# Kernel optimization log

Measured on AMD Instinct MI355X. Metric: run time of the kernel, lower is better.

## Reference

```python
import jax, jax.numpy as jnp
import numpy as np
from jax import lax

# Architecture constants (match init_kwargs)
B = 4          # clips
T_SEG = 8      # num_segments
D_IN = 256
D_HID = 64
H = 112
W = 112
WIN_T = 5      # window[0], temporal
WIN_S = 9      # window[1] == window[2], spatial
MAXD = WIN_S // 2


def setup_inputs() -> dict:
    key = jax.random.key(0)
    k1, k2, k3, k4 = jax.random.split(key, 4)
    x = jax.random.normal(k1, (B * T_SEG, D_IN, H, W), jnp.float32)
    conv_w = jax.random.normal(k2, (D_HID, D_IN, 3, 3), jnp.float32) * 0.05
    bn_gamma = jnp.ones((D_HID,), jnp.float32)
    bn_beta = jnp.zeros((D_HID,), jnp.float32)
    bn_mean = jax.random.normal(k3, (D_HID,), jnp.float32) * 0.1
    bn_var = jax.random.uniform(k4, (D_HID,), jnp.float32, minval=0.5, maxval=1.5)
    return {"x": x, "conv_w": conv_w, "bn_gamma": bn_gamma, "bn_beta": bn_beta,
            "bn_mean": bn_mean, "bn_var": bn_var}


def reference(x, conv_w, bn_gamma, bn_beta, bn_mean, bn_var):
    # downsample: Conv2d(k=3, s=2, p=1, no bias) + BatchNorm2d (eval) + ReLU
    y = lax.conv_general_dilated(x, conv_w, window_strides=(2, 2),
                                 padding=((1, 1), (1, 1)),
                                 dimension_numbers=("NCHW", "OIHW", "NCHW"))
    scale = bn_gamma / jnp.sqrt(bn_var + 1e-5)
    y = jax.nn.relu((y - bn_mean[:, None, None]) * scale[:, None, None]
                    + bn_beta[:, None, None])
    bt, c, h, w = y.shape
    b = bt // T_SEG
    y = y.reshape(b, T_SEG, c, h, w)
    # per-frame, per-pixel L2 normalization over channels (eps=1e-6, as in _L2normalize)
    yn = y / jnp.sqrt(jnp.sum(y * y, axis=2, keepdims=True) + 1e-6)
    # temporal zero-pad (padded frames normalize to 0 in the original too: 0/sqrt(eps)=0)
    half_t = WIN_T // 2
    ypad = jnp.pad(yn, ((0, 0), (half_t, half_t), (0, 0), (0, 0), (0, 0)))
    # spatial zero-pad by max displacement
    ypad = jnp.pad(ypad, ((0, 0), (0, 0), (0, 0), (MAXD, MAXD), (MAXD, MAXD)))
    # temporal windows: f2[b, t, l] = padded frame t+l   -> (b, T, L, c, h+2m, w+2m)
    f2 = jnp.stack([ypad[:, l:l + T_SEG] for l in range(WIN_T)], axis=2)
    # local windowed correlation (equivalent to einsum + _corr_abs_to_rel):
    # out[b,t,l,u,v,h,w] = sum_c yn[b,t,c,h,w] * f2[b,t,l,c,h+u,w+v]
    corrs = []
    for u in range(WIN_S):
        for v in range(WIN_S):
            corrs.append(jnp.einsum("btchw,btlchw->btlhw",
                                     yn, f2[:, :, :, :, u:u + h, v:v + w]))
    corr = jnp.stack(corrs, axis=-1).reshape(b, T_SEG, WIN_T, h, w, WIN_S, WIN_S)
    # '(b t l) u v h w -> b t h w 1 l u v'
    corr = jnp.transpose(corr, (0, 1, 3, 4, 2, 5, 6))
    return corr[:, :, :, :, None, :, :, :]
```

## Files before the change

### kernel.cpp

```cpp
#include <hip/hip_runtime.h>
#include <hip/hip_bf16.h>

#define TSEG 8
#define NBC 4
#define NBT 32
#define CIN 256
#define CH 64
#define HIN 112
#define WIN_ 112
#define HO 56
#define WO 56
#define HPD 64
#define WPD 64

#define FRSZE ((size_t)(HPD * WPD * CH))
#define ZF_U   147456
#define FR_U   (ZF_U + 262144)
#define WS_TOTAL_BYTES ((size_t)(FR_U + 32 * 262144) * 2)

typedef __attribute__((ext_vector_type(8))) short bf16x8;
typedef __attribute__((ext_vector_type(4))) float f32x4;

__device__ __forceinline__ unsigned short f2bf(float f) {
    union { float f; unsigned u; } c; c.f = f;
    unsigned u = c.u + 0x7fffu + ((c.u >> 16) & 1u);
    return (unsigned short)(u >> 16);
}

__global__ __launch_bounds__(256) void wprep_k(
    const float* __restrict__ w, unsigned short* __restrict__ wpp)
{
    int e = blockIdx.x * 256 + threadIdx.x;
    int cout = e / 2304;
    int rem  = e - cout * 2304;
    int ci   = rem / 9;
    int tap  = rem - ci * 9;
    wpp[((size_t)tap * 64 + cout) * 256 + ci] = f2bf(w[e]);
}

__global__ __launch_bounds__(256) void conv_mfma_k(
    const float* __restrict__ x, const unsigned short* __restrict__ wpp,
    const float* __restrict__ gamma, const float* __restrict__ beta,
    const float* __restrict__ mean, const float* __restrict__ var,
    unsigned short* __restrict__ frames)
{
    __shared__ unsigned short in_lds[5 * 120 * 32];
    __shared__ float sq[2][2][64];

    const int tid  = threadIdx.x;
    const int lane = tid & 63;
    const int wv   = tid >> 6;
    const int r    = wv >> 1;
    const int nh   = wv & 1;
    const int l15  = lane & 15;
    const int l4   = lane >> 4;
    const int hb   = blockIdx.x;
    const int bt   = blockIdx.y;

    const float* xb = x + (size_t)bt * (CIN * HIN * WIN_);

    f32x4 acc[4][2];
#pragma unroll
    for (int mt = 0; mt < 4; ++mt) {
        acc[mt][0] = (f32x4){0.f, 0.f, 0.f, 0.f};
        acc[mt][1] = (f32x4){0.f, 0.f, 0.f, 0.f};
    }

    int a_off[4][3];
#pragma unroll
    for (int mt = 0; mt < 4; ++mt) {
        int c = mt * 16 + l15; if (c > 55) c = 55;
#pragma unroll
        for (int kw = 0; kw < 3; ++kw) {
            int col = 2 * c + kw;
            int ba  = col * 64 + l4 * 16;
            ba ^= ((col >> 1) & 7) << 4;
            a_off[mt][kw] = ba;
        }
    }

    const unsigned short* bptr0 = wpp + ((size_t)(nh * 32 + l15) * 256 + l4 * 8);
    const unsigned short* bptr1 = wpp + ((size_t)(nh * 32 + 16 + l15) * 256 + l4 * 8);

    const int ih0 = 4 * hb - 1;

    for (int cb = 0; cb < 8; ++cb) {
        __syncthreads();
#pragma unroll
        for (int j = 0; j < 5; ++j) {
            const int jj  = wv + j * 4;
            const int row = jj >> 2, cig = jj & 3;
            const int ih  = ih0 + row;
            const int ihc = ih < 0 ? 0 : (ih > 111 ? 111 : ih);
            const float* xr = xb + ((size_t)(cb * 32 + cig * 8) * HIN + ihc) * WIN_;
            const bool rowin = (ih >= 0) && (ih < HIN);
#pragma unroll
            for (int p = 0; p < 2; ++p) {
                const int col = lane + p * 64;
                if (col < 113) {
                    const int iw  = col - 1;
                    const int iwc = iw < 0 ? 0 : iw;
                    const bool inb = rowin && (iw >= 0);
                    unsigned pk[4];
#pragma unroll
                    for (int q = 0; q < 4; ++q) {
                        float v0 = xr[(size_t)(2 * q) * HIN * WIN_ + iwc];
                        float v1 = xr[(size_t)(2 * q + 1) * HIN * WIN_ + iwc];
                        v0 = inb ? v0 : 0.f;
                        v1 = inb ? v1 : 0.f;
                        union { float f; unsigned u; } c0, c1; c0.f = v0; c1.f = v1;
                        unsigned u0 = c0.u + 0x7fffu + ((c0.u >> 16) & 1u);
                        unsigned u1 = c1.u + 0x7fffu + ((c1.u >> 16) & 1u);
                        pk[q] = (u0 >> 16) | (u1 & 0xffff0000u);
                    }
                    int ba = (row * 120 + col) * 64 + cig * 16;
                    ba ^= ((col >> 1) & 7) << 4;
                    *(uint4*)((char*)in_lds + ba) = make_uint4(pk[0], pk[1], pk[2], pk[3]);
                }
            }
        }
        __syncthreads();

        const int rowb = (2 * r) * 7680;
#pragma unroll
        for (int kh = 0; kh < 3; ++kh) {
            const int rb = rowb + kh * 7680;
#pragma unroll
            for (int kw = 0; kw < 3; ++kw) {
                const int tap = kh * 3 + kw;
                const bf16x8 bf0 = *(const bf16x8*)(bptr0 + tap * 16384 + cb * 32);
                const bf16x8 bf1 = *(const bf16x8*)(bptr1 + tap * 16384 + cb * 32);
#pragma unroll
                for (int mt = 0; mt < 4; ++mt) {
                    const bf16x8 af = *(const bf16x8*)((const char*)in_lds + (rb + a_off[mt][kw]));
                    acc[mt][0] = __builtin_amdgcn_mfma_f32_16x16x32_bf16(af, bf0, acc[mt][0], 0, 0, 0);
                    acc[mt][1] = __builtin_amdgcn_mfma_f32_16x16x32_bf16(af, bf1, acc[mt][1], 0, 0, 0);
                }
            }
        }
    }

    const int cout0 = nh * 32 + l15;
    const int cout1 = cout0 + 16;
    const float sc0 = gamma[cout0] * rsqrtf(var[cout0] + 1e-5f);
    const float bb0 = beta[cout0] - mean[cout0] * sc0;
    const float sc1 = gamma[cout1] * rsqrtf(var[cout1] + 1e-5f);
    const float bb1 = beta[cout1] - mean[cout1] * sc1;

    float yv[4][2][4];
    float ssr[4][4];
#pragma unroll
    for (int mt = 0; mt < 4; ++mt) {
#pragma unroll
        for (int reg = 0; reg < 4; ++reg) {
            float y0 = fmaxf(fmaf(acc[mt][0][reg], sc0, bb0), 0.f);
            float y1 = fmaxf(fmaf(acc[mt][1][reg], sc1, bb1), 0.f);
            yv[mt][0][reg] = y0; yv[mt][1][reg] = y1;
            float ss = y0 * y0 + y1 * y1;
            ss += __shfl_xor(ss, 1);
            ss += __shfl_xor(ss, 2);
            ss += __shfl_xor(ss, 4);
            ss += __shfl_xor(ss, 8);
            ssr[mt][reg] = ss;
        }
    }
    if (l15 == 0) {
#pragma unroll
        for (int mt = 0; mt < 4; ++mt)
#pragma unroll
            for (int reg = 0; reg < 4; ++reg)
                sq[r][nh][mt * 16 + l4 * 4 + reg] = ssr[mt][reg];
    }
    __syncthreads();

    const int h = 2 * hb + r;
    unsigned short* fdst = frames + (size_t)bt * FRSZE + (size_t)(h + 4) * WPD * CH;
#pragma unroll
    for (int mt = 0; mt < 4; ++mt) {
#pragma unroll
        for (int reg = 0; reg < 4; ++reg) {
            const int c = mt * 16 + l4 * 4 + reg;
            if (c < 56) {
                const float tot = sq[r][0][c] + sq[r][1][c];
                const float inv = rsqrtf(tot + 1e-6f);
                unsigned short* dp = fdst + (size_t)(c + 4) * CH;
                dp[cout0] = f2bf(yv[mt][0][reg] * inv);
                dp[cout1] = f2bf(yv[mt][1][reg] * inv);
            }
        }
    }
}

__global__ __launch_bounds__(64) void corr_mfma_k(
    const unsigned short* __restrict__ frames, float* __restrict__ out)
{
    __shared__ float so[56 * 84];

    const int lane = threadIdx.x;
    const int l15  = lane & 15;
    const int l4   = lane >> 4;
    const int h    = blockIdx.x;
    const int tl   = blockIdx.y;
    const int t    = tl / 5;
    const int l    = tl - 5 * t;
    const int b    = blockIdx.z;
    const int bt   = b * TSEG + t;

    float* ob = out + (size_t)(bt * HO + h) * (WO * 405) + l * 81;

    const int f = t + l;
    if (f < 2 || f > 9) {
#pragma unroll
        for (int w = 0; w < 56; ++w) {
            float* orow = ob + (size_t)w * 405;
            orow[lane] = 0.f;
            if (lane < 17) orow[lane + 64] = 0.f;
        }
        return;
    }

    const unsigned short* yrow = frames + (size_t)bt * FRSZE + (size_t)(h + 4) * (WPD * CH);
    bf16x8 af[4][2];
#pragma unroll
    for (int m = 0; m < 4; ++m) {
        int w = (m << 4) + l15; if (w > 55) w = 55;
        const unsigned short* ap = yrow + (size_t)(w + 4) * CH + (l4 << 3);
        af[m][0] = *(const bf16x8*)(ap);
        af[m][1] = *(const bf16x8*)(ap + 32);
    }

    const unsigned short* zb = frames + (size_t)(b * TSEG + f - 2) * FRSZE
                             + (size_t)h * (WPD * CH);

    const int PM[7] = {0, 0, 1, 1, 2, 2, 3};
    const int PN[7] = {0, 1, 1, 2, 2, 3, 3};

#define LOADB(buf, uu) { \
    const unsigned short* zr = zb + (size_t)(uu) * (WPD * CH); \
    _Pragma("unroll") \
    for (int n = 0; n < 4; ++n) { \
        const unsigned short* bp = zr + (size_t)((n << 4) + l15) * CH + (l4 << 3); \
        buf[n][0] = *(const bf16x8*)(bp); \
        buf[n][1] = *(const bf16x8*)(bp + 32); } }

#define COMPU(buf, uu) { \
    f32x4 acc[7]; \
    _Pragma("unroll") \
    for (int i = 0; i < 7; ++i) acc[i] = (f32x4){0.f, 0.f, 0.f, 0.f}; \
    _Pragma("unroll") \
    for (int i = 0; i < 7; ++i) { \
        acc[i] = __builtin_amdgcn_mfma_f32_16x16x32_bf16(af[PM[i]][0], buf[PN[i]][0], acc[i], 0, 0, 0); \
        acc[i] = __builtin_amdgcn_mfma_f32_16x16x32_bf16(af[PM[i]][1], buf[PN[i]][1], acc[i], 0, 0, 0); } \
    _Pragma("unroll") \
    for (int i = 0; i < 7; ++i) { \
        const int zc = (PN[i] << 4) + l15; \
        const int w0 = (PM[i] << 4) + (l4 << 2); \
        _Pragma("unroll") \
        for (int rr = 0; rr < 4; ++rr) { \
            const int w = w0 + rr; \
            const int v = zc - w; \
            if (w < 56 && (unsigned)v <= 8u) \
                so[w * 84 + (uu) * 9 + v] = acc[i][rr]; } } }

    bf16x8 b0[4][2], b1[4][2], b2[4][2];
    LOADB(b0, 0); LOADB(b1, 1);
    LOADB(b2, 2); COMPU(b0, 0);
    LOADB(b0, 3); COMPU(b1, 1);
    LOADB(b1, 4); COMPU(b2, 2);
    LOADB(b2, 5); COMPU(b0, 3);
    LOADB(b0, 6); COMPU(b1, 4);
    LOADB(b1, 7); COMPU(b2, 5);
    LOADB(b2, 8); COMPU(b0, 6);
    COMPU(b1, 7);
    COMPU(b2, 8);

#undef LOADB
#undef COMPU

#pragma unroll
    for (int w = 0; w < 56; ++w) {
        const float* sr = so + w * 84;
        float* orow = ob + (size_t)w * 405;
        orow[lane] = sr[lane];
        if (lane < 17) orow[lane + 64] = sr[lane + 64];
    }
}

extern "C" void kernel_launch(void* const* d_in, const int* in_sizes, int n_in,
                              void* d_out, int out_size, void* d_ws, size_t ws_size,
                              hipStream_t stream)
{
    const float* x     = (const float*)d_in[0];
    const float* wgt   = (const float*)d_in[1];
    const float* gamma = (const float*)d_in[2];
    const float* beta  = (const float*)d_in[3];
    const float* mean  = (const float*)d_in[4];
    const float* var   = (const float*)d_in[5];
    float* out = (float*)d_out;

    unsigned short* wpp    = (unsigned short*)d_ws;
    unsigned short* frames = wpp + FR_U;

    if (ws_size < WS_TOTAL_BYTES) return;

    hipMemsetAsync(d_ws, 0, WS_TOTAL_BYTES, stream);
    wprep_k<<<dim3(576), 256, 0, stream>>>(wgt, wpp);
    conv_mfma_k<<<dim3(28, NBT), 256, 0, stream>>>(x, wpp, gamma, beta, mean, var, frames);
    corr_mfma_k<<<dim3(56, 40, NBC), 64, 0, stream>>>(frames, out);
}
```

Before: 274.7 us.

## Process two output rows per correlation block and remap block IDs across XCDs

The correlation kernel now computes two adjacent output rows per block. Each loaded row of the padded neighbour frame feeds both query rows, which cuts B-fragment global loads by about half and halves the block count. Both kernels also remap the linear block ID with a stride-8 swizzle so that consecutive work lands on the same XCD, which should improve L2 locality on MI355X. The cost is twice the LDS staging buffer and more live registers, which may lower occupancy.

```diff
diff --git a/kernel.cpp b/kernel.cpp
--- a/kernel.cpp
+++ b/kernel.cpp
@@ -54,8 +54,11 @@
     const int nh   = wv & 1;
     const int l15  = lane & 15;
     const int l4   = lane >> 4;
-    const int hb   = blockIdx.x;
-    const int bt   = blockIdx.y;
+
+    const int bid = blockIdx.x + 28 * blockIdx.y;
+    const int L   = (bid & 7) * 112 + (bid >> 3);
+    const int hb  = L % 28;
+    const int bt  = L / 28;
 
     const float* xb = x + (size_t)bt * (CIN * HIN * WIN_);
 
@@ -194,95 +197,113 @@
 __global__ __launch_bounds__(64) void corr_mfma_k(
     const unsigned short* __restrict__ frames, float* __restrict__ out)
 {
-    __shared__ float so[56 * 84];
+    __shared__ float so[2 * 56 * 84];
 
     const int lane = threadIdx.x;
     const int l15  = lane & 15;
     const int l4   = lane >> 4;
-    const int h    = blockIdx.x;
-    const int tl   = blockIdx.y;
-    const int t    = tl / 5;
-    const int l    = tl - 5 * t;
-    const int b    = blockIdx.z;
-    const int bt   = b * TSEG + t;
-
-    float* ob = out + (size_t)(bt * HO + h) * (WO * 405) + l * 81;
+
+    const int bid = blockIdx.x;
+    const int L   = (bid & 7) * 560 + (bid >> 3);
+    const int hp  = L % 28;
+    const int rem = L / 28;
+    const int tl  = rem % 40;
+    const int b   = rem / 40;
+    const int t   = tl / 5, l = tl - 5 * t;
+    const int h0  = hp * 2;
+    const int bt  = b * TSEG + t;
+
+    float* ob0 = out + (size_t)(bt * HO + h0) * (WO * 405) + l * 81;
 
     const int f = t + l;
     if (f < 2 || f > 9) {
 #pragma unroll
-        for (int w = 0; w < 56; ++w) {
-            float* orow = ob + (size_t)w * 405;
-            orow[lane] = 0.f;
-            if (lane < 17) orow[lane + 64] = 0.f;
+        for (int hh = 0; hh < 2; ++hh) {
+            float* ob = ob0 + (size_t)hh * (WO * 405);
+#pragma unroll 4
+            for (int w = 0; w < 56; ++w) {
+                float* orow = ob + (size_t)w * 405;
+                orow[lane] = 0.f;
+                if (lane < 17) orow[lane + 64] = 0.f;
+            }
         }
         return;
     }
 
-    const unsigned short* yrow = frames + (size_t)bt * FRSZE + (size_t)(h + 4) * (WPD * CH);
-    bf16x8 af[4][2];
-#pragma unroll
-    for (int m = 0; m < 4; ++m) {
-        int w = (m << 4) + l15; if (w > 55) w = 55;
-        const unsigned short* ap = yrow + (size_t)(w + 4) * CH + (l4 << 3);
-        af[m][0] = *(const bf16x8*)(ap);
-        af[m][1] = *(const bf16x8*)(ap + 32);
+    bf16x8 af[2][4][2];
+#pragma unroll
+    for (int hh = 0; hh < 2; ++hh) {
+        const unsigned short* yrow = frames + (size_t)bt * FRSZE
+                                   + (size_t)(h0 + hh + 4) * (WPD * CH);
+#pragma unroll
+        for (int m = 0; m < 4; ++m) {
+            int w = (m << 4) + l15; if (w > 55) w = 55;
+            const unsigned short* ap = yrow + (size_t)(w + 4) * CH + (l4 << 3);
+            af[hh][m][0] = *(const bf16x8*)(ap);
+            af[hh][m][1] = *(const bf16x8*)(ap + 32);
+        }
     }
 
     const unsigned short* zb = frames + (size_t)(b * TSEG + f - 2) * FRSZE
-                             + (size_t)h * (WPD * CH);
+                             + (size_t)h0 * (WPD * CH);
 
     const int PM[7] = {0, 0, 1, 1, 2, 2, 3};
     const int PN[7] = {0, 1, 1, 2, 2, 3, 3};
 
-#define LOADB(buf, uu) { \
-    const unsigned short* zr = zb + (size_t)(uu) * (WPD * CH); \
+#define LOADB(buf, rr) { \
+    const unsigned short* zr = zb + (size_t)(rr) * (WPD * CH); \
     _Pragma("unroll") \
     for (int n = 0; n < 4; ++n) { \
         const unsigned short* bp = zr + (size_t)((n << 4) + l15) * CH + (l4 << 3); \
         buf[n][0] = *(const bf16x8*)(bp); \
         buf[n][1] = *(const bf16x8*)(bp + 32); } }
 
-#define COMPU(buf, uu) { \
+#define COMPU(buf, hh, uu) { \
     f32x4 acc[7]; \
     _Pragma("unroll") \
     for (int i = 0; i < 7; ++i) acc[i] = (f32x4){0.f, 0.f, 0.f, 0.f}; \
     _Pragma("unroll") \
     for (int i = 0; i < 7; ++i) { \
-        acc[i] = __builtin_amdgcn_mfma_f32_16x16x32_bf16(af[PM[i]][0], buf[PN[i]][0], acc[i], 0, 0, 0); \
-        acc[i] = __builtin_amdgcn_mfma_f32_16x16x32_bf16(af[PM[i]][1], buf[PN[i]][1], acc[i], 0, 0, 0); } \
+        acc[i] = __builtin_amdgcn_mfma_f32_16x16x32_bf16(af[hh][PM[i]][0], buf[PN[i]][0], acc[i], 0, 0, 0); \
+        acc[i] = __builtin_amdgcn_mfma_f32_16x16x32_bf16(af[hh][PM[i]][1], buf[PN[i]][1], acc[i], 0, 0, 0); } \
     _Pragma("unroll") \
     for (int i = 0; i < 7; ++i) { \
         const int zc = (PN[i] << 4) + l15; \
         const int w0 = (PM[i] << 4) + (l4 << 2); \
         _Pragma("unroll") \
-        for (int rr = 0; rr < 4; ++rr) { \
-            const int w = w0 + rr; \
+        for (int rr2 = 0; rr2 < 4; ++rr2) { \
+            const int w = w0 + rr2; \
             const int v = zc - w; \
             if (w < 56 && (unsigned)v <= 8u) \
-                so[w * 84 + (uu) * 9 + v] = acc[i][rr]; } } }
+                so[(hh) * 4704 + w * 84 + (uu) * 9 + v] = acc[i][rr2]; } } }
 
     bf16x8 b0[4][2], b1[4][2], b2[4][2];
-    LOADB(b0, 0); LOADB(b1, 1);
-    LOADB(b2, 2); COMPU(b0, 0);
-    LOADB(b0, 3); COMPU(b1, 1);
-    LOADB(b1, 4); COMPU(b2, 2);
-    LOADB(b2, 5); COMPU(b0, 3);
-    LOADB(b0, 6); COMPU(b1, 4);
-    LOADB(b1, 7); COMPU(b2, 5);
-    LOADB(b2, 8); COMPU(b0, 6);
-    COMPU(b1, 7);
-    COMPU(b2, 8);
+    LOADB(b0, 0); LOADB(b1, 1); LOADB(b2, 2);
+    COMPU(b0, 0, 0);                    LOADB(b0, 3);
+    COMPU(b1, 0, 1); COMPU(b1, 1, 0);   LOADB(b1, 4);
+    COMPU(b2, 0, 2); COMPU(b2, 1, 1);   LOADB(b2, 5);
+    COMPU(b0, 0, 3); COMPU(b0, 1, 2);   LOADB(b0, 6);
+    COMPU(b1, 0, 4); COMPU(b1, 1, 3);   LOADB(b1, 7);
+    COMPU(b2, 0, 5); COMPU(b2, 1, 4);   LOADB(b2, 8);
+    COMPU(b0, 0, 6); COMPU(b0, 1, 5);   LOADB(b0, 9);
+    COMPU(b1, 0, 7); COMPU(b1, 1, 6);
+    COMPU(b2, 0, 8); COMPU(b2, 1, 7);
+    COMPU(b0, 1, 8);
 
 #undef LOADB
 #undef COMPU
 
 #pragma unroll
-    for (int w = 0; w < 56; ++w) {
-        const float* sr = so + w * 84;
-        float* orow = ob + (size_t)w * 405;
-        orow[lane] = sr[lane];
-        if (lane < 17) orow[lane + 64] = sr[lane + 64];
+    for (int hh = 0; hh < 2; ++hh) {
+        float* ob = ob0 + (size_t)hh * (WO * 405);
+        const float* sb = so + hh * 4704;
+#pragma unroll 4
+        for (int w = 0; w < 56; ++w) {
+            const float* sr = sb + w * 84;
+            float* orow = ob + (size_t)w * 405;
+            orow[lane] = sr[lane];
+            if (lane < 17) orow[lane + 64] = sr[lane + 64];
+        }
     }
 }
 
@@ -306,5 +327,5 @@
     hipMemsetAsync(d_ws, 0, WS_TOTAL_BYTES, stream);
     wprep_k<<<dim3(576), 256, 0, stream>>>(wgt, wpp);
     conv_mfma_k<<<dim3(28, NBT), 256, 0, stream>>>(x, wpp, gamma, beta, mean, var, frames);
-    corr_mfma_k<<<dim3(56, 40, NBC), 64, 0, stream>>>(frames, out);
-}
+    corr_mfma_k<<<dim3(4480), 64, 0, stream>>>(frames, out);
+}
```

After: 291.8 us. 6.2% more time.

## Stage correlation frame rows in a rolling LDS window shared across output rows

Applied to the files above, without the earlier changes.

The correlation kernel now gives each block a strip of 14 output rows. It keeps a 12-slot ring buffer of padded frame rows in LDS with an XOR swizzle, so the 9 vertical displacements reuse staged rows instead of each output row reloading all 9 rows from global memory. Two waves process alternating rows, and the next row's global loads are overlapped with the current row's MFMA work, synchronised by barriers. The cost is more LDS per block (about 134 KB), which lowers occupancy, plus barrier synchronisation, in exchange for much less redundant global traffic.

```diff
diff --git a/kernel.cpp b/kernel.cpp
--- a/kernel.cpp
+++ b/kernel.cpp
@@ -12,6 +12,7 @@
 #define WO 56
 #define HPD 64
 #define WPD 64
+#define NSLOT 12
 
 #define FRSZE ((size_t)(HPD * WPD * CH))
 #define ZF_U   147456
@@ -191,99 +192,174 @@
     }
 }
 
-__global__ __launch_bounds__(64) void corr_mfma_k(
+__global__ __launch_bounds__(128) void corr_roll_k(
     const unsigned short* __restrict__ frames, float* __restrict__ out)
 {
-    __shared__ float so[56 * 84];
-
-    const int lane = threadIdx.x;
+    __shared__ unsigned short win[NSLOT * 4096];
+    __shared__ float so[2][56 * 84];
+
+    const int tid  = threadIdx.x;
+    const int lane = tid & 63;
+    const int wv   = tid >> 6;
     const int l15  = lane & 15;
     const int l4   = lane >> 4;
-    const int h    = blockIdx.x;
-    const int tl   = blockIdx.y;
-    const int t    = tl / 5;
-    const int l    = tl - 5 * t;
-    const int b    = blockIdx.z;
-    const int bt   = b * TSEG + t;
-
-    float* ob = out + (size_t)(bt * HO + h) * (WO * 405) + l * 81;
+
+    const int bid   = blockIdx.x;
+    const int unit  = bid >> 2;
+    const int strip = bid & 3;
+    const int b  = unit / 40;
+    const int rm = unit - b * 40;
+    const int t  = rm / 5;
+    const int l  = rm - t * 5;
+    const int h0 = strip * 14;
+    const int bt = b * TSEG + t;
+
+    float* obase = out + (size_t)(bt * HO) * (WO * 405) + l * 81;
 
     const int f = t + l;
     if (f < 2 || f > 9) {
 #pragma unroll
-        for (int w = 0; w < 56; ++w) {
-            float* orow = ob + (size_t)w * 405;
-            orow[lane] = 0.f;
-            if (lane < 17) orow[lane + 64] = 0.f;
+        for (int i = 0; i < 7; ++i) {
+            const int h = h0 + 2 * i + wv;
+            float* ob = obase + (size_t)h * (WO * 405);
+#pragma unroll 4
+            for (int w = 0; w < 56; ++w) {
+                float* orow = ob + (size_t)w * 405;
+                orow[lane] = 0.f;
+                if (lane < 17) orow[lane + 64] = 0.f;
+            }
         }
         return;
     }
 
-    const unsigned short* yrow = frames + (size_t)bt * FRSZE + (size_t)(h + 4) * (WPD * CH);
-    bf16x8 af[4][2];
-#pragma unroll
-    for (int m = 0; m < 4; ++m) {
-        int w = (m << 4) + l15; if (w > 55) w = 55;
-        const unsigned short* ap = yrow + (size_t)(w + 4) * CH + (l4 << 3);
-        af[m][0] = *(const bf16x8*)(ap);
-        af[m][1] = *(const bf16x8*)(ap + 32);
-    }
-
-    const unsigned short* zb = frames + (size_t)(b * TSEG + f - 2) * FRSZE
-                             + (size_t)h * (WPD * CH);
+    const unsigned short* fb = frames + (size_t)(b * TSEG + f - 2) * FRSZE;
+    const unsigned short* cf = frames + (size_t)bt * FRSZE;
+
+    int woff[8];
+#pragma unroll
+    for (int q = 0; q < 8; ++q)
+        woff[q] = (q * 1024 + lane * 16) ^ (((lane >> 3) & 7) << 4);
+
+    int roff[4][2];
+#pragma unroll
+    for (int n = 0; n < 4; ++n) {
+        const int px = n * 16 + l15;
+#pragma unroll
+        for (int hf = 0; hf < 2; ++hf)
+            roff[n][hf] = (px * 128 + hf * 64 + l4 * 16) ^ ((px & 7) << 4);
+    }
 
     const int PM[7] = {0, 0, 1, 1, 2, 2, 3};
     const int PN[7] = {0, 1, 1, 2, 2, 3, 3};
 
-#define LOADB(buf, uu) { \
-    const unsigned short* zr = zb + (size_t)(uu) * (WPD * CH); \
+#define STAGE_LOAD(g, row) { \
+    const unsigned short* zr = fb + (size_t)(row) * 4096 + lane * 8; \
     _Pragma("unroll") \
-    for (int n = 0; n < 4; ++n) { \
-        const unsigned short* bp = zr + (size_t)((n << 4) + l15) * CH + (l4 << 3); \
-        buf[n][0] = *(const bf16x8*)(bp); \
-        buf[n][1] = *(const bf16x8*)(bp + 32); } }
-
-#define COMPU(buf, uu) { \
-    f32x4 acc[7]; \
+    for (int q = 0; q < 8; ++q) g[q] = *(const uint4*)(zr + q * 512); }
+
+#define STAGE_WRITE(g, row) { \
+    char* wb = (char*)win + ((row) % NSLOT) * 8192; \
     _Pragma("unroll") \
-    for (int i = 0; i < 7; ++i) acc[i] = (f32x4){0.f, 0.f, 0.f, 0.f}; \
+    for (int q = 0; q < 8; ++q) *(uint4*)(wb + woff[q]) = g[q]; }
+
+#define LOADA(af, hh) { \
+    const unsigned short* yr = cf + (size_t)((hh) + 4) * 4096; \
     _Pragma("unroll") \
-    for (int i = 0; i < 7; ++i) { \
-        acc[i] = __builtin_amdgcn_mfma_f32_16x16x32_bf16(af[PM[i]][0], buf[PN[i]][0], acc[i], 0, 0, 0); \
-        acc[i] = __builtin_amdgcn_mfma_f32_16x16x32_bf16(af[PM[i]][1], buf[PN[i]][1], acc[i], 0, 0, 0); } \
+    for (int m = 0; m < 4; ++m) { \
+        int w = (m << 4) + l15; if (w > 55) w = 55; \
+        const unsigned short* ap = yr + (w + 4) * 64 + (l4 << 3); \
+        af[m][0] = *(const bf16x8*)(ap); \
+        af[m][1] = *(const bf16x8*)(ap + 32); } }
+
+#define COMPH(af, hh) { \
+    float* sw = so[wv]; \
+    const int hm = (hh) % NSLOT; \
     _Pragma("unroll") \
-    for (int i = 0; i < 7; ++i) { \
-        const int zc = (PN[i] << 4) + l15; \
-        const int w0 = (PM[i] << 4) + (l4 << 2); \
+    for (int u = 0; u < 9; ++u) { \
+        int sl = hm + u; if (sl >= NSLOT) sl -= NSLOT; \
+        const char* rb = (const char*)win + sl * 8192; \
+        bf16x8 bfr[4][2]; \
         _Pragma("unroll") \
-        for (int rr = 0; rr < 4; ++rr) { \
-            const int w = w0 + rr; \
-            const int v = zc - w; \
-            if (w < 56 && (unsigned)v <= 8u) \
-                so[w * 84 + (uu) * 9 + v] = acc[i][rr]; } } }
-
-    bf16x8 b0[4][2], b1[4][2], b2[4][2];
-    LOADB(b0, 0); LOADB(b1, 1);
-    LOADB(b2, 2); COMPU(b0, 0);
-    LOADB(b0, 3); COMPU(b1, 1);
-    LOADB(b1, 4); COMPU(b2, 2);
-    LOADB(b2, 5); COMPU(b0, 3);
-    LOADB(b0, 6); COMPU(b1, 4);
-    LOADB(b1, 7); COMPU(b2, 5);
-    LOADB(b2, 8); COMPU(b0, 6);
-    COMPU(b1, 7);
-    COMPU(b2, 8);
-
-#undef LOADB
-#undef COMPU
-
-#pragma unroll
-    for (int w = 0; w < 56; ++w) {
-        const float* sr = so + w * 84;
-        float* orow = ob + (size_t)w * 405;
-        orow[lane] = sr[lane];
-        if (lane < 17) orow[lane + 64] = sr[lane + 64];
-    }
+        for (int n = 0; n < 4; ++n) { \
+            bfr[n][0] = *(const bf16x8*)(rb + roff[n][0]); \
+            bfr[n][1] = *(const bf16x8*)(rb + roff[n][1]); } \
+        f32x4 acc[7]; \
+        _Pragma("unroll") \
+        for (int i = 0; i < 7; ++i) acc[i] = (f32x4){0.f, 0.f, 0.f, 0.f}; \
+        _Pragma("unroll") \
+        for (int i = 0; i < 7; ++i) { \
+            acc[i] = __builtin_amdgcn_mfma_f32_16x16x32_bf16(af[PM[i]][0], bfr[PN[i]][0], acc[i], 0, 0, 0); \
+            acc[i] = __builtin_amdgcn_mfma_f32_16x16x32_bf16(af[PM[i]][1], bfr[PN[i]][1], acc[i], 0, 0, 0); } \
+        _Pragma("unroll") \
+        for (int i = 0; i < 7; ++i) { \
+            const int zc = (PN[i] << 4) + l15; \
+            const int w0 = (PM[i] << 4) + (l4 << 2); \
+            _Pragma("unroll") \
+            for (int rr = 0; rr < 4; ++rr) { \
+                const int w = w0 + rr; \
+                const int v = zc - w; \
+                if (w < 56 && (unsigned)v <= 8u) \
+                    sw[w * 84 + u * 9 + v] = acc[i][rr]; } } } }
+
+#define STORES(hh) { \
+    float* ob = obase + (size_t)(hh) * (WO * 405); \
+    const float* sb = so[wv]; \
+    _Pragma("unroll 4") \
+    for (int w = 0; w < 56; ++w) { \
+        const float* sr = sb + w * 84; \
+        float* orow = ob + (size_t)w * 405; \
+        orow[lane] = sr[lane]; \
+        if (lane < 17) orow[lane + 64] = sr[lane + 64]; } }
+
+    bf16x8 A0[4][2], A1[4][2];
+    {
+        uint4 ga[8], gb[8];
+        STAGE_LOAD(ga, h0 + wv + 0);
+        STAGE_LOAD(gb, h0 + wv + 2);
+        STAGE_WRITE(ga, h0 + wv + 0);
+        STAGE_LOAD(ga, h0 + wv + 4);
+        STAGE_WRITE(gb, h0 + wv + 2);
+        STAGE_LOAD(gb, h0 + wv + 6);
+        STAGE_WRITE(ga, h0 + wv + 4);
+        STAGE_LOAD(ga, h0 + wv + 8);
+        STAGE_WRITE(gb, h0 + wv + 6);
+        STAGE_WRITE(ga, h0 + wv + 8);
+        LOADA(A0, h0 + wv);
+        asm volatile("s_waitcnt lgkmcnt(0)" ::: "memory");
+        __builtin_amdgcn_sched_barrier(0);
+        __builtin_amdgcn_s_barrier();
+    }
+
+    uint4 gs[8];
+#define STEP(s, AC, AN) { \
+    const int h_ = h0 + 2 * (s) + wv; \
+    if ((s) < 6) { \
+        STAGE_LOAD(gs, h0 + 2 * (s) + 10 + wv); \
+        LOADA(AN, h0 + 2 * ((s) + 1) + wv); \
+    } \
+    COMPH(AC, h_); \
+    if ((s) < 6) { \
+        STAGE_WRITE(gs, h0 + 2 * (s) + 10 + wv); \
+        asm volatile("s_waitcnt lgkmcnt(0)" ::: "memory"); \
+        __builtin_amdgcn_sched_barrier(0); \
+        __builtin_amdgcn_s_barrier(); \
+    } \
+    STORES(h_); }
+
+    STEP(0, A0, A1);
+    STEP(1, A1, A0);
+    STEP(2, A0, A1);
+    STEP(3, A1, A0);
+    STEP(4, A0, A1);
+    STEP(5, A1, A0);
+    STEP(6, A0, A1);
+
+#undef STEP
+#undef STORES
+#undef COMPH
+#undef LOADA
+#undef STAGE_WRITE
+#undef STAGE_LOAD
 }
 
 extern "C" void kernel_launch(void* const* d_in, const int* in_sizes, int n_in,
@@ -306,5 +382,5 @@
     hipMemsetAsync(d_ws, 0, WS_TOTAL_BYTES, stream);
     wprep_k<<<dim3(576), 256, 0, stream>>>(wgt, wpp);
     conv_mfma_k<<<dim3(28, NBT), 256, 0, stream>>>(x, wpp, gamma, beta, mean, var, frames);
-    corr_mfma_k<<<dim3(56, 40, NBC), 64, 0, stream>>>(frames, out);
-}
+    corr_roll_k<<<dim3(640), 128, 0, stream>>>(frames, out);
+}
```

After: 881.5 us. +220.9%, slower.

## Halve correlation LDS staging and flush output in two phases for occupancy

Applied to the files above, without the earlier changes.

Shrinks the per-block shared staging buffer to hold only half the displacement rows, writing the first five u-rows to global memory before computing the rest and reusing the buffer. Drops one B-fragment register buffer (triple to double buffering) and adds a launch-bounds occupancy hint, with partial unrolling of store loops. Aims to raise waves per CU on this memory/LDS-bound kernel, at the cost of less load latency hiding and narrower output store phases.

```diff
diff --git a/kernel.cpp b/kernel.cpp
--- a/kernel.cpp
+++ b/kernel.cpp
@@ -191,10 +191,11 @@
     }
 }
 
-__global__ __launch_bounds__(64) void corr_mfma_k(
+#define SSTR 45
+__global__ __launch_bounds__(64, 4) void corr_mfma_k(
     const unsigned short* __restrict__ frames, float* __restrict__ out)
 {
-    __shared__ float so[56 * 84];
+    __shared__ float so[56 * SSTR];
 
     const int lane = threadIdx.x;
     const int l15  = lane & 15;
@@ -210,7 +211,7 @@
 
     const int f = t + l;
     if (f < 2 || f > 9) {
-#pragma unroll
+#pragma unroll 4
         for (int w = 0; w < 56; ++w) {
             float* orow = ob + (size_t)w * 405;
             orow[lane] = 0.f;
@@ -244,6 +245,7 @@
         buf[n][1] = *(const bf16x8*)(bp + 32); } }
 
 #define COMPU(buf, uu) { \
+    const int ucol = ((uu) < 5) ? (uu) * 9 : ((uu) - 5) * 9; \
     f32x4 acc[7]; \
     _Pragma("unroll") \
     for (int i = 0; i < 7; ++i) acc[i] = (f32x4){0.f, 0.f, 0.f, 0.f}; \
@@ -260,30 +262,33 @@
             const int w = w0 + rr; \
             const int v = zc - w; \
             if (w < 56 && (unsigned)v <= 8u) \
-                so[w * 84 + (uu) * 9 + v] = acc[i][rr]; } } }
-
-    bf16x8 b0[4][2], b1[4][2], b2[4][2];
+                so[w * SSTR + ucol + v] = acc[i][rr]; } } }
+
+    bf16x8 b0[4][2], b1[4][2];
     LOADB(b0, 0); LOADB(b1, 1);
-    LOADB(b2, 2); COMPU(b0, 0);
-    LOADB(b0, 3); COMPU(b1, 1);
-    LOADB(b1, 4); COMPU(b2, 2);
-    LOADB(b2, 5); COMPU(b0, 3);
-    LOADB(b0, 6); COMPU(b1, 4);
-    LOADB(b1, 7); COMPU(b2, 5);
-    LOADB(b2, 8); COMPU(b0, 6);
+    COMPU(b0, 0); LOADB(b0, 2);
+    COMPU(b1, 1); LOADB(b1, 3);
+    COMPU(b0, 2); LOADB(b0, 4);
+    COMPU(b1, 3); LOADB(b1, 5);
+    COMPU(b0, 4); LOADB(b0, 6);
+
+#pragma unroll 4
+    for (int w = 0; w < 56; ++w) {
+        if (lane < 45) ob[(size_t)w * 405 + lane] = so[w * SSTR + lane];
+    }
+
+    COMPU(b1, 5); LOADB(b1, 7);
+    COMPU(b0, 6); LOADB(b0, 8);
     COMPU(b1, 7);
-    COMPU(b2, 8);
+    COMPU(b0, 8);
+
+#pragma unroll 4
+    for (int w = 0; w < 56; ++w) {
+        if (lane < 36) ob[(size_t)w * 405 + 45 + lane] = so[w * SSTR + lane];
+    }
 
 #undef LOADB
 #undef COMPU
-
-#pragma unroll
-    for (int w = 0; w < 56; ++w) {
-        const float* sr = so + w * 84;
-        float* orow = ob + (size_t)w * 405;
-        orow[lane] = sr[lane];
-        if (lane < 17) orow[lane + 64] = sr[lane + 64];
-    }
 }
 
 extern "C" void kernel_launch(void* const* d_in, const int* in_sizes, int n_in,
```

After: 338.1 us. +23.1%, slower.
